# Kernel optimization log

Measured on AMD Instinct MI355X. Metric: run time of the kernel, lower is better.

The kernel has to match this reference:

```python
import jax, jax.numpy as jnp
import numpy as np

N = 200000   # 10000 graphs x 20 nodes, stacked
E = 3200000  # avg degree 16
F_IN = 4
H = 32
BN_EPS = 1e-5


def setup_inputs() -> dict:
    key = jax.random.key(0)
    ks = jax.random.split(key, 16)
    s = 0.1
    return {
        "x": jax.random.normal(ks[0], (N, F_IN), jnp.float32),
        "edge_index": jax.random.randint(ks[1], (2, E), 0, N, jnp.int64),
        "edge_weight": jax.random.uniform(ks[2], (E,), jnp.float32),
        "gcn1_w": jax.random.normal(ks[3], (F_IN, H), jnp.float32) * s,
        "gcn1_b": jnp.zeros((H,), jnp.float32),
        "gcn2_w": jax.random.normal(ks[4], (H, H), jnp.float32) * s,
        "gcn2_b": jnp.zeros((H,), jnp.float32),
        "bn1_gamma": jnp.ones((H,), jnp.float32),
        "bn1_beta": jnp.zeros((H,), jnp.float32),
        "bn1_mean": jnp.zeros((H,), jnp.float32),
        "bn1_var": jnp.ones((H,), jnp.float32),
        "bn2_gamma": jnp.ones((H,), jnp.float32),
        "bn2_beta": jnp.zeros((H,), jnp.float32),
        "bn2_mean": jnp.zeros((H,), jnp.float32),
        "bn2_var": jnp.ones((H,), jnp.float32),
        "lstm1_wih": jax.random.normal(ks[5], (4 * H, 2 * H), jnp.float32) * s,
        "lstm1_whh": jax.random.normal(ks[6], (4 * H, H), jnp.float32) * s,
        "lstm1_bih": jax.random.normal(ks[7], (4 * H,), jnp.float32) * s,
        "lstm1_bhh": jax.random.normal(ks[8], (4 * H,), jnp.float32) * s,
        "lstm2_wih": jax.random.normal(ks[9], (4 * H, H), jnp.float32) * s,
        "lstm2_whh": jax.random.normal(ks[10], (4 * H, H), jnp.float32) * s,
        "lstm2_bih": jax.random.normal(ks[11], (4 * H,), jnp.float32) * s,
        "lstm2_bhh": jax.random.normal(ks[12], (4 * H,), jnp.float32) * s,
        "lin_w": jax.random.normal(ks[13], (1, 2 * H + F_IN), jnp.float32) * s,
        "lin_b": jnp.zeros((1,), jnp.float32),
    }


def _gcn_conv(x, src, dst, ew, W, b, n):
    # GCNConv: x @ W, add self-loops (weight 1), symmetric normalization, scatter-add at dst.
    xw = x @ W
    loop = jnp.arange(n)
    s = jnp.concatenate([src, loop])
    d = jnp.concatenate([dst, loop])
    w = jnp.concatenate([ew, jnp.ones((n,), ew.dtype)])
    deg = jax.ops.segment_sum(w, d, num_segments=n)
    dinv = jnp.where(deg > 0, jax.lax.rsqrt(deg), 0.0)
    norm = dinv[s] * w * dinv[d]  # [E+N]
    out = jax.ops.segment_sum(norm[:, None] * xw[s], d, num_segments=n)
    return out + b


def _bn_eval(x, gamma, beta, mean, var):
    return (x - mean) * jax.lax.rsqrt(var + BN_EPS) * gamma + beta


def _lstm_step(x, wih, bih, bhh):
    # single timestep, zero initial (h, c): recurrent W_hh term vanishes.
    gates = x @ wih.T + bih + bhh
    i, f, g, o = jnp.split(gates, 4, axis=1)  # torch gate order i,f,g,o
    c = jax.nn.sigmoid(i) * jnp.tanh(g)
    return jax.nn.sigmoid(o) * jnp.tanh(c)


def reference(x, edge_index, edge_weight, gcn1_w, gcn1_b, gcn2_w, gcn2_b,
              bn1_gamma, bn1_beta, bn1_mean, bn1_var,
              bn2_gamma, bn2_beta, bn2_mean, bn2_var,
              lstm1_wih, lstm1_whh, lstm1_bih, lstm1_bhh,
              lstm2_wih, lstm2_whh, lstm2_bih, lstm2_bhh,
              lin_w, lin_b):
    n = x.shape[0]
    src, dst = edge_index[0], edge_index[1]
    # MPNNLSTM (window=1, eval mode: dropout=identity, BN uses running stats)
    h1 = _bn_eval(jax.nn.relu(_gcn_conv(x, src, dst, edge_weight, gcn1_w, gcn1_b, n)),
                  bn1_gamma, bn1_beta, bn1_mean, bn1_var)
    h2 = _bn_eval(jax.nn.relu(_gcn_conv(h1, src, dst, edge_weight, gcn2_w, gcn2_b, n)),
                  bn2_gamma, bn2_beta, bn2_mean, bn2_var)
    skip = jnp.concatenate([h1, h2], axis=1)  # [N, 2H]
    H1 = _lstm_step(skip, lstm1_wih, lstm1_bih, lstm1_bhh)  # [N, H]
    H2 = _lstm_step(H1, lstm2_wih, lstm2_bih, lstm2_bhh)    # [N, H]
    h = jnp.concatenate([H1, H2, x], axis=1)  # [N, 2H + F_IN]
    # RecurrentGCN head: relu + linear -> [N, 1]
    return jax.nn.relu(h) @ lin_w.T + lin_b
```

## Files before the change

kernel.cpp:

```cpp
#include <hip/hip_runtime.h>
#include <hip/hip_fp16.h>
#include <math.h>

#define BN_EPS 1e-5f
#define HF 32
#define BS 256
#define KEDGE 4096
#define MAXNB 800
#define WQ14 16383.0f
#define WQ22 4194303.0f

typedef _Float16 half8 __attribute__((ext_vector_type(8)));
typedef float f32x4 __attribute__((ext_vector_type(4)));
typedef float f32x2 __attribute__((ext_vector_type(2)));

__device__ __forceinline__ float fsig(float x) {
    return __builtin_amdgcn_rcpf(1.0f + __expf(-x));
}
__device__ __forceinline__ float ftanh(float x) {
    return 1.0f - 2.0f * __builtin_amdgcn_rcpf(1.0f + __expf(2.0f * x));
}


__device__ __forceinline__ float e4m3_to_f32_sw(unsigned v) {
    unsigned s = v & 0x80u, E = (v >> 3) & 0xFu, m = v & 7u;
    float r = E ? ldexpf((float)(8 + m), (int)E - 10) : ldexpf((float)m, -9);
    return s ? -r : r;
}

__device__ __forceinline__ unsigned f32_to_e4m3_sw(float x) {
    float ax = fabsf(x);
    unsigned s = x < 0.0f ? 0x80u : 0u;
    if (!(ax > 0.0f)) return s;
    if (ax >= 448.0f) return s | 0x7Eu;
    int e;
    float m = frexpf(ax, &e);
    int E = e - 1 + 7;
    if (E >= 1) {
        int q = (int)(m * 16.0f + 0.5f);
        if (q == 16) { q = 8; E += 1; if (E > 15) return s | 0x7Eu; }
        return s | (unsigned)(E << 3) | (unsigned)(q - 8);
    }
    int q = (int)(ax * 512.0f + 0.5f);
    if (q > 7) return s | 0x08u;
    return s | (unsigned)q;
}

__device__ __forceinline__ void dec8(uint2 r, float* f) {
#if __has_builtin(__builtin_amdgcn_cvt_pk_f32_fp8)
    f32x2 p0 = __builtin_amdgcn_cvt_pk_f32_fp8((int)r.x, false);
    f32x2 p1 = __builtin_amdgcn_cvt_pk_f32_fp8((int)r.x, true);
    f32x2 p2 = __builtin_amdgcn_cvt_pk_f32_fp8((int)r.y, false);
    f32x2 p3 = __builtin_amdgcn_cvt_pk_f32_fp8((int)r.y, true);
    f[0] = p0[0]; f[1] = p0[1]; f[2] = p1[0]; f[3] = p1[1];
    f[4] = p2[0]; f[5] = p2[1]; f[6] = p3[0]; f[7] = p3[1];
#else
#pragma unroll
    for (int k = 0; k < 4; ++k) f[k] = e4m3_to_f32_sw((r.x >> (8 * k)) & 0xFFu);
#pragma unroll
    for (int k = 0; k < 4; ++k) f[4 + k] = e4m3_to_f32_sw((r.y >> (8 * k)) & 0xFFu);
#endif
}

__device__ __forceinline__ uint2 enc8(const float* o) {
#if __has_builtin(__builtin_amdgcn_cvt_pk_fp8_f32)
    int w0 = 0, w1 = 0;
    w0 = __builtin_amdgcn_cvt_pk_fp8_f32(o[0], o[1], w0, false);
    w0 = __builtin_amdgcn_cvt_pk_fp8_f32(o[2], o[3], w0, true);
    w1 = __builtin_amdgcn_cvt_pk_fp8_f32(o[4], o[5], w1, false);
    w1 = __builtin_amdgcn_cvt_pk_fp8_f32(o[6], o[7], w1, true);
    return make_uint2((unsigned)w0, (unsigned)w1);
#else
    unsigned a = 0, b = 0;
#pragma unroll
    for (int k = 0; k < 4; ++k) a |= f32_to_e4m3_sw(o[k]) << (8 * k);
#pragma unroll
    for (int k = 0; k < 4; ++k) b |= f32_to_e4m3_sw(o[4 + k]) << (8 * k);
    return make_uint2(a, b);
#endif
}


__global__ __launch_bounds__(512) void k_binsort(
        const int* __restrict__ src, const int* __restrict__ dst,
        const float* __restrict__ ew, int E, int NB, int bcap,
        int* __restrict__ gcur, uint2* __restrict__ recs) {
    __shared__ uint2 srec[KEDGE];
    __shared__ int hist[MAXNB], excl[MAXNB], curs[MAXNB], sbase[MAXNB];

    int tid = threadIdx.x;
    int base = blockIdx.x * KEDGE;
    int cnt = min(KEDGE, E - base);

    for (int i = tid; i < NB; i += 512) hist[i] = 0;
    __syncthreads();

    for (int i = tid; i < cnt; i += 512)
        atomicAdd(&hist[dst[base + i] >> 8], 1);
    __syncthreads();

    if (tid < 64) {
        int run = 0;
        for (int c = 0; c < NB; c += 64) {
            int idx = c + tid;
            int v = (idx < NB) ? hist[idx] : 0;
            int incl = v;
#pragma unroll
            for (int o = 1; o < 64; o <<= 1) {
                int up = __shfl_up(incl, o, 64);
                if (tid >= o) incl += up;
            }
            if (idx < NB) { int e = run + incl - v; excl[idx] = e; curs[idx] = e; }
            run += __shfl(incl, 63, 64);
        }
    }
    __syncthreads();

    for (int i = tid; i < cnt; i += 512) {
        int s = src[base + i];
        int d = dst[base + i];
        float w = ew[base + i];
        unsigned q = (unsigned)(w * WQ22 + 0.5f);
        if (q > 4194303u) q = 4194303u;
        int b = d >> 8;
        int pos = atomicAdd(&curs[b], 1);
        srec[pos] = make_uint2(((unsigned)s << 8) | (unsigned)(d & 255),
                               ((unsigned)b << 22) | q);
    }
    __syncthreads();

    for (int b = tid; b < NB; b += 512) {
        int len = hist[b];
        sbase[b] = len ? atomicAdd(&gcur[b], len) : 0;
    }
    __syncthreads();

    for (int i = tid; i < cnt; i += 512) {
        uint2 u = srec[i];
        int b = u.y >> 22;
        int off = sbase[b] + (i - excl[b]);
        if (off < bcap) recs[(size_t)b * bcap + off] = u;
    }
}


__global__ __launch_bounds__(512) void k_sortb(
        const uint2* __restrict__ recs, const int* __restrict__ gcur, int bcap,
        unsigned* __restrict__ recs4, int* __restrict__ pstart,
        int* __restrict__ pcnt, float* __restrict__ dinv, int n) {
    __shared__ int hist[BS], excl[BS], curs[BS];
    __shared__ float wsum[BS];

    int b = blockIdx.x, tid = threadIdx.x;
    int cnt = min(gcur[b], bcap);
    const uint2* r = recs + (size_t)b * bcap;
    const float dq = 1.0f / WQ22;

    if (tid < BS) { hist[tid] = 0; wsum[tid] = 1.0f; }
    __syncthreads();

    for (int i = tid; i < cnt; i += 512) {
        uint2 u = r[i];
        int dl = u.x & 255;
        atomicAdd(&hist[dl], 1);
        atomicAdd(&wsum[dl], (float)(u.y & 4194303u) * dq);
    }
    __syncthreads();

    if (tid < BS) wsum[tid] = rsqrtf(wsum[tid]);
    if (tid < 64) {
        int run = 0;
        for (int c = 0; c < BS; c += 64) {
            int idx = c + tid;
            int v = hist[idx];
            int incl = v;
#pragma unroll
            for (int o = 1; o < 64; o <<= 1) {
                int up = __shfl_up(incl, o, 64);
                if (tid >= o) incl += up;
            }
            int e = run + incl - v;
            excl[idx] = e; curs[idx] = e;
            run += __shfl(incl, 63, 64);
        }
    }
    __syncthreads();

    unsigned* out4 = recs4 + (size_t)b * bcap;
    for (int i = tid; i < cnt; i += 512) {
        uint2 u = r[i];
        int dl = u.x & 255;
        int pos = atomicAdd(&curs[dl], 1);
        float qn = (float)(u.y & 4194303u) * dq * wsum[dl];
        unsigned q = (unsigned)(qn * WQ14 + 0.5f);
        if (q > 16383u) q = 16383u;
        out4[pos] = ((u.x >> 8) << 14) | q;
    }

    if (tid < BS) {
        int g = b * BS + tid;
        if (g < n) {
            pstart[g] = b * bcap + excl[tid];
            pcnt[g] = hist[tid];
            dinv[g] = wsum[tid];
        }
    }
}


__global__ __launch_bounds__(256) void k_prep(
        const float* __restrict__ wih1, const float* __restrict__ bih1,
        const float* __restrict__ bhh1, const float* __restrict__ wih2,
        const float* __restrict__ bih2, const float* __restrict__ bhh2,
        __half* __restrict__ wp1, __half* __restrict__ wp2,
        float* __restrict__ bsum1, float* __restrict__ bsum2,
        int* __restrict__ gcur, int NB,
        const float* __restrict__ x, const float* __restrict__ W1,
        unsigned char* __restrict__ y18, int n) {
    const int tg[6] = {0, 16, 64, 80, 96, 112};
    __shared__ float sW[128];
    int tid = threadIdx.x;
    if (tid < 128) sW[tid] = W1[tid];
    __syncthreads();

    int idx = blockIdx.x * 256 + tid;
    if (idx < 6144) {
        int t = idx >> 10, rem = idx & 1023;
        int kc = rem >> 9, rem2 = rem & 511;
        int lane = rem2 >> 3, j = rem2 & 7;
        int g = tg[t] + (lane & 15);
        int k = kc * 32 + (lane >> 4) * 8 + j;
        wp1[idx] = __float2half(wih1[g * 64 + k]);
    } else if (idx < 9216) {
        int i2 = idx - 6144;
        int t = i2 >> 9, rem2 = i2 & 511;
        int lane = rem2 >> 3, j = rem2 & 7;
        int g = tg[t] + (lane & 15);
        int k = (lane >> 4) * 8 + j;
        wp2[i2] = __float2half(wih2[g * 32 + k]);
    } else if (idx < 9344) {
        int i = idx - 9216;
        bsum1[i] = bih1[i] + bhh1[i];
    } else if (idx < 9472) {
        int i = idx - 9344;
        bsum2[i] = bih2[i] + bhh2[i];
    } else if (idx < 9472 + NB) {
        gcur[idx - 9472] = 0;
    } else if (idx >= 16384) {
        int j = idx - 16384;
        int node = j >> 2, lane = j & 3;
        if (node < n) {
            float4 xv = *(const float4*)(x + (size_t)node * 4);
            int fq = lane * 8;
            float o[8];
#pragma unroll
            for (int k = 0; k < 8; ++k)
                o[k] = xv.x * sW[fq + k] + xv.y * sW[32 + fq + k] +
                       xv.z * sW[64 + fq + k] + xv.w * sW[96 + fq + k];
            ((uint2*)(y18 + ((size_t)node << 5)))[lane] = enc8(o);
        }
    }
}


__global__ __launch_bounds__(256) void k_g1w2(
        const unsigned* __restrict__ recs4, const int* __restrict__ pstart,
        const int* __restrict__ pcnt, const float* __restrict__ dinv,
        const unsigned char* __restrict__ y18, const float* __restrict__ W2,
        const float* __restrict__ bias, const float* __restrict__ gamma,
        const float* __restrict__ beta, const float* __restrict__ mean,
        const float* __restrict__ var,
        __half* __restrict__ skiph, unsigned char* __restrict__ A8, int n) {
    __shared__ float sW2[1024];
    __shared__ float sh1[64][33];
    int tid = threadIdx.x;
    for (int i = tid; i < 1024; i += 256) sW2[i] = W2[i];
    __syncthreads();

    int nl = tid >> 2;
    int g = blockIdx.x * 64 + nl;
    int lane = tid & 3;
    int fq = lane * 8;
    bool act = g < n;

    float acc[8];
#pragma unroll
    for (int k = 0; k < 8; ++k) acc[k] = 0.0f;

    if (act) {
        float dig = dinv[g];
        float sl = dig * dig;
        {
            uint2 sr = ((const uint2*)(y18 + ((size_t)g << 5)))[lane];
            float f[8];
            dec8(sr, f);
#pragma unroll
            for (int k = 0; k < 8; ++k) acc[k] = sl * f[k];
        }

        const float qs = 1.0f / WQ14;
        int cn = pcnt[g];
        const unsigned* r = recs4 + pstart[g];
        int e = 0;
        for (; e + 8 <= cn; e += 8) {
            unsigned u[8];
            uint2 rw[8];
            float nm[8];
#pragma unroll
            for (int q = 0; q < 8; ++q) u[q] = r[e + q];
#pragma unroll
            for (int q = 0; q < 8; ++q)
                rw[q] = ((const uint2*)(y18 + ((size_t)(u[q] >> 14) << 5)))[lane];
#pragma unroll
            for (int q = 0; q < 8; ++q)
                nm[q] = (float)(u[q] & 16383u) * qs * dinv[u[q] >> 14];
#pragma unroll
            for (int q = 0; q < 8; ++q) {
                float f[8];
                dec8(rw[q], f);
#pragma unroll
                for (int k = 0; k < 8; ++k) acc[k] += nm[q] * f[k];
            }
        }
        for (; e < cn; ++e) {
            unsigned u0 = r[e];
            uint2 r0 = ((const uint2*)(y18 + ((size_t)(u0 >> 14) << 5)))[lane];
            float n0 = (float)(u0 & 16383u) * qs * dinv[u0 >> 14];
            float f[8];
            dec8(r0, f);
#pragma unroll
            for (int k = 0; k < 8; ++k) acc[k] += n0 * f[k];
        }
    }

    float o[8];
#pragma unroll
    for (int k = 0; k < 8; ++k) {
        float v = fmaxf(acc[k] + bias[fq + k], 0.0f);
        o[k] = (v - mean[fq + k]) * gamma[fq + k] * rsqrtf(var[fq + k] + BN_EPS) + beta[fq + k];
        sh1[nl][fq + k] = o[k];
    }
    if (act) {
        union { __half h[8]; uint4 q; } hv;
#pragma unroll
        for (int k = 0; k < 8; ++k) hv.h[k] = __float2half(o[k]);
        *(uint4*)(skiph + (size_t)g * 64 + fq) = hv.q;
    }
    __syncthreads();

    if (act) {
        float a2[8];
#pragma unroll
        for (int j = 0; j < 8; ++j) a2[j] = 0.0f;
#pragma unroll 4
        for (int k = 0; k < 32; ++k) {
            float h = sh1[nl][k];
            const float* wr = sW2 + k * 32 + fq;
#pragma unroll
            for (int j = 0; j < 8; ++j) a2[j] += h * wr[j];
        }
        ((uint2*)(A8 + ((size_t)g << 5)))[lane] = enc8(a2);
    }
}


__global__ __launch_bounds__(256) void k_gather8(
        const unsigned* __restrict__ recs4, const int* __restrict__ pstart,
        const int* __restrict__ pcnt, const float* __restrict__ dinv,
        const unsigned char* __restrict__ A8,
        const float* __restrict__ bias, const float* __restrict__ gamma,
        const float* __restrict__ beta, const float* __restrict__ mean,
        const float* __restrict__ var,
        __half* __restrict__ skiph, int uoff, int n) {
    int g = blockIdx.x * 64 + (threadIdx.x >> 2);
    int lane = threadIdx.x & 3;
    if (g >= n) return;

    float dig = dinv[g];
    float sl = dig * dig;
    float acc[8];
    {
        uint2 sr = ((const uint2*)(A8 + ((size_t)g << 5)))[lane];
        float f[8];
        dec8(sr, f);
#pragma unroll
        for (int k = 0; k < 8; ++k) acc[k] = sl * f[k];
    }

    const float qs = 1.0f / WQ14;
    int cn = pcnt[g];
    const unsigned* r = recs4 + pstart[g];
    int e = 0;
    for (; e + 8 <= cn; e += 8) {
        unsigned u[8];
        uint2 rw[8];
        float nm[8];
#pragma unroll
        for (int q = 0; q < 8; ++q) u[q] = r[e + q];
#pragma unroll
        for (int q = 0; q < 8; ++q)
            rw[q] = ((const uint2*)(A8 + ((size_t)(u[q] >> 14) << 5)))[lane];
#pragma unroll
        for (int q = 0; q < 8; ++q)
            nm[q] = (float)(u[q] & 16383u) * qs * dinv[u[q] >> 14];
#pragma unroll
        for (int q = 0; q < 8; ++q) {
            float f[8];
            dec8(rw[q], f);
#pragma unroll
            for (int k = 0; k < 8; ++k) acc[k] += nm[q] * f[k];
        }
    }
    for (; e < cn; ++e) {
        unsigned u0 = r[e];
        uint2 r0 = ((const uint2*)(A8 + ((size_t)(u0 >> 14) << 5)))[lane];
        float n0 = (float)(u0 & 16383u) * qs * dinv[u0 >> 14];
        float f0[8];
        dec8(r0, f0);
#pragma unroll
        for (int k = 0; k < 8; ++k) acc[k] += n0 * f0[k];
    }

    int fq = lane * 8;
    union { __half h[8]; uint4 q; } hv;
#pragma unroll
    for (int k = 0; k < 8; ++k) {
        float v = fmaxf(acc[k] + bias[fq + k], 0.0f);
        hv.h[k] = __float2half((v - mean[fq + k]) * gamma[fq + k] * rsqrtf(var[fq + k] + BN_EPS) + beta[fq + k]);
    }
    *(uint4*)(skiph + (size_t)g * 64 + uoff + fq) = hv.q;
}


__global__ __launch_bounds__(256) void k_headm(
        const __half* __restrict__ skiph, const float* __restrict__ x,
        const __half* __restrict__ wp1, const __half* __restrict__ wp2,
        const float* __restrict__ bsum1, const float* __restrict__ bsum2,
        const float* __restrict__ lw, const float* __restrict__ lb,
        float* __restrict__ out, int n) {
    __shared__ __align__(16) __half H1lds[4 * 16 * 40];
    int tid = threadIdx.x;
    int w = tid >> 6, l = tid & 63;
    int quad = l >> 4, c = l & 15;
    int node_base = blockIdx.x * 64 + w * 16;

    int arow = node_base + c; if (arow > n - 1) arow = n - 1;
    const half8* ap = (const half8*)(skiph + (size_t)arow * 64);
    half8 a0 = ap[quad];
    half8 a1 = ap[4 + quad];

    const half8* b1 = (const half8*)wp1;
    f32x4 d[6];
#pragma unroll
    for (int t = 0; t < 6; ++t) {
        f32x4 acc = {0.0f, 0.0f, 0.0f, 0.0f};
        acc = __builtin_amdgcn_mfma_f32_16x16x32_f16(a0, b1[(t * 2 + 0) * 64 + l], acc, 0, 0, 0);
        acc = __builtin_amdgcn_mfma_f32_16x16x32_f16(a1, b1[(t * 2 + 1) * 64 + l], acc, 0, 0, 0);
        d[t] = acc;
    }

    float bi0 = bsum1[c],      bi1 = bsum1[16 + c];
    float bg0 = bsum1[64 + c], bg1 = bsum1[80 + c];
    float bo0 = bsum1[96 + c], bo1 = bsum1[112 + c];
    float lwc0 = lw[c], lwc1 = lw[c + 16];

    float pa[4];
#pragma unroll
    for (int r = 0; r < 4; ++r) {
        float cc0 = fsig(d[0][r] + bi0) * ftanh(d[2][r] + bg0);
        float h0 = fsig(d[4][r] + bo0) * ftanh(cc0);
        float cc1 = fsig(d[1][r] + bi1) * ftanh(d[3][r] + bg1);
        float h1 = fsig(d[5][r] + bo1) * ftanh(cc1);
        pa[r] = fmaxf(h0, 0.0f) * lwc0 + fmaxf(h1, 0.0f) * lwc1;
        __half* hp = H1lds + (w * 16 + quad * 4 + r) * 40;
        hp[c] = __float2half(h0);
        hp[c + 16] = __float2half(h1);
    }
    __syncthreads();

    half8 a2 = *(const half8*)(H1lds + (w * 16 + c) * 40 + quad * 8);

    const half8* b2 = (const half8*)wp2;
    f32x4 e[6];
#pragma unroll
    for (int t = 0; t < 6; ++t) {
        f32x4 acc = {0.0f, 0.0f, 0.0f, 0.0f};
        e[t] = __builtin_amdgcn_mfma_f32_16x16x32_f16(a2, b2[t * 64 + l], acc, 0, 0, 0);
    }

    float ci0 = bsum2[c],      ci1 = bsum2[16 + c];
    float cg0 = bsum2[64 + c], cg1 = bsum2[80 + c];
    float co0 = bsum2[96 + c], co1 = bsum2[112 + c];
    float lw2c0 = lw[32 + c], lw2c1 = lw[48 + c];
#pragma unroll
    for (int r = 0; r < 4; ++r) {
        float cc0 = fsig(e[0][r] + ci0) * ftanh(e[2][r] + cg0);
        float h0 = fsig(e[4][r] + co0) * ftanh(cc0);
        float cc1 = fsig(e[1][r] + ci1) * ftanh(e[3][r] + cg1);
        float h1 = fsig(e[5][r] + co1) * ftanh(cc1);
        pa[r] += fmaxf(h0, 0.0f) * lw2c0 + fmaxf(h1, 0.0f) * lw2c1;
    }

#pragma unroll
    for (int m = 1; m < 16; m <<= 1) {
#pragma unroll
        for (int r = 0; r < 4; ++r) pa[r] += __shfl_xor(pa[r], m, 64);
    }

    if (c < 4) {
        int node = node_base + quad * 4 + c;
        if (node < n) {
            const float4 xv = *(const float4*)(x + (size_t)node * 4);
            out[node] = pa[c] + lb[0]
                + fmaxf(xv.x, 0.0f) * lw[64] + fmaxf(xv.y, 0.0f) * lw[65]
                + fmaxf(xv.z, 0.0f) * lw[66] + fmaxf(xv.w, 0.0f) * lw[67];
        }
    }
}


__global__ void k_initdeg(float* __restrict__ deg, int n) {
    int i = blockIdx.x * blockDim.x + threadIdx.x;
    if (i < n) deg[i] = 1.0f;
}

__global__ void k_deg_only(const int* __restrict__ dst, const float* __restrict__ ew,
                           float* __restrict__ deg, int E) {
    int e = blockIdx.x * blockDim.x + threadIdx.x;
    if (e < E) atomicAdd(&deg[dst[e]], ew[e]);
}

__global__ void k_dinv_f(float* __restrict__ deg, int n) {
    int i = blockIdx.x * blockDim.x + threadIdx.x;
    if (i < n) {
        float d = deg[i];
        deg[i] = d > 0.0f ? rsqrtf(d) : 0.0f;
    }
}

__global__ void k_xw1_f(const float* __restrict__ x, const float* __restrict__ W,
                        float* __restrict__ out, int n) {
    int idx = blockIdx.x * blockDim.x + threadIdx.x;
    if (idx >= n * HF) return;
    int nn = idx >> 5, f = idx & 31;
    const float4 xr = *(const float4*)(x + (size_t)nn * 4);
    out[idx] = xr.x * W[f] + xr.y * W[32 + f] + xr.z * W[64 + f] + xr.w * W[96 + f];
}

__global__ void k_xw2_f(const float* __restrict__ Hin, const float* __restrict__ W,
                        float* __restrict__ out, int n) {
    __shared__ float sW[32 * 32];
    __shared__ float sH[8][32];
    int tid = threadIdx.x;
    for (int i = tid; i < 1024; i += 256) sW[i] = W[i];
    int r = tid >> 5, f = tid & 31;
    int nn = blockIdx.x * 8 + r;
    if (nn < n) sH[r][f] = Hin[(size_t)nn * HF + f];
    __syncthreads();
    if (nn >= n) return;
    float acc = 0.0f;
#pragma unroll
    for (int k = 0; k < 32; ++k) acc += sH[r][k] * sW[k * 32 + f];
    out[(size_t)nn * HF + f] = acc;
}

__global__ void k_selfloop(const float* __restrict__ A, const float* __restrict__ dinv,
                           float* __restrict__ B, int n) {
    int idx = blockIdx.x * blockDim.x + threadIdx.x;
    if (idx >= n * HF) return;
    int nn = idx >> 5;
    float di = dinv[nn];
    B[idx] = di * di * A[idx];
}

__global__ void k_scatter(const int* __restrict__ src, const int* __restrict__ dst,
                          const float* __restrict__ ew, const float* __restrict__ dinv,
                          const float* __restrict__ A, float* __restrict__ B, int total) {
    int idx = blockIdx.x * blockDim.x + threadIdx.x;
    if (idx >= total) return;
    int e = idx >> 5, f = idx & 31;
    int s = src[e], d = dst[e];
    float norm = dinv[s] * ew[e] * dinv[d];
    atomicAdd(&B[d * HF + f], norm * A[s * HF + f]);
}

__global__ void k_post(const float* __restrict__ B, const float* __restrict__ bias,
                       const float* __restrict__ gamma, const float* __restrict__ beta,
                       const float* __restrict__ mean, const float* __restrict__ var,
                       float* __restrict__ Hout, int n) {
    int idx = blockIdx.x * blockDim.x + threadIdx.x;
    if (idx >= n * HF) return;
    int f = idx & 31;
    float v = fmaxf(B[idx] + bias[f], 0.0f);
    float sc = gamma[f] * rsqrtf(var[f] + BN_EPS);
    Hout[idx] = (v - mean[f]) * sc + beta[f];
}

__global__ __launch_bounds__(256) void k_head(
        const float* __restrict__ h1, const float* __restrict__ h2,
        const float* __restrict__ x,
        const float* __restrict__ wih1, const float* __restrict__ bih1, const float* __restrict__ bhh1,
        const float* __restrict__ wih2, const float* __restrict__ bih2, const float* __restrict__ bhh2,
        const float* __restrict__ lw, const float* __restrict__ lb,
        float* __restrict__ out, int n) {
    __shared__ float sH1[32 * 256];
    int tid = threadIdx.x;
    int nn = blockIdx.x * 256 + tid;
    if (nn >= n) return;

    const float4* a = (const float4*)(h1 + (size_t)nn * HF);
    const float4* b = (const float4*)(h2 + (size_t)nn * HF);
    float skip[64];
#pragma unroll
    for (int q = 0; q < 8; ++q) {
        float4 v = a[q];
        skip[4 * q] = v.x; skip[4 * q + 1] = v.y; skip[4 * q + 2] = v.z; skip[4 * q + 3] = v.w;
        float4 u = b[q];
        skip[32 + 4 * q] = u.x; skip[33 + 4 * q] = u.y; skip[34 + 4 * q] = u.z; skip[35 + 4 * q] = u.w;
    }

    float oa = lb[0];
#pragma unroll 1
    for (int j = 0; j < 32; ++j) {
        const float4* wi = (const float4*)(wih1 + (size_t)j * 64);
        const float4* wg = (const float4*)(wih1 + (size_t)(64 + j) * 64);
        const float4* wo = (const float4*)(wih1 + (size_t)(96 + j) * 64);
        float gi = bih1[j] + bhh1[j];
        float gg = bih1[64 + j] + bhh1[64 + j];
        float go = bih1[96 + j] + bhh1[96 + j];
#pragma unroll
        for (int q = 0; q < 16; ++q) {
            float4 aa = wi[q], bb = wg[q], cc4 = wo[q];
            float s0 = skip[4 * q], s1 = skip[4 * q + 1], s2 = skip[4 * q + 2], s3 = skip[4 * q + 3];
            gi += aa.x * s0 + aa.y * s1 + aa.z * s2 + aa.w * s3;
            gg += bb.x * s0 + bb.y * s1 + bb.z * s2 + bb.w * s3;
            go += cc4.x * s0 + cc4.y * s1 + cc4.z * s2 + cc4.w * s3;
        }
        float cc = fsig(gi) * ftanh(gg);
        float hh = fsig(go) * ftanh(cc);
        sH1[j * 256 + tid] = hh;
        oa += fmaxf(hh, 0.0f) * lw[j];
    }

#pragma unroll 1
    for (int j = 0; j < 32; ++j) {
        const float4* wi = (const float4*)(wih2 + (size_t)j * 32);
        const float4* wg = (const float4*)(wih2 + (size_t)(64 + j) * 32);
        const float4* wo = (const float4*)(wih2 + (size_t)(96 + j) * 32);
        float gi = bih2[j] + bhh2[j];
        float gg = bih2[64 + j] + bhh2[64 + j];
        float go = bih2[96 + j] + bhh2[96 + j];
#pragma unroll
        for (int q = 0; q < 8; ++q) {
            float4 aa = wi[q], bb = wg[q], cc4 = wo[q];
            float s0 = sH1[(4 * q) * 256 + tid], s1 = sH1[(4 * q + 1) * 256 + tid];
            float s2 = sH1[(4 * q + 2) * 256 + tid], s3 = sH1[(4 * q + 3) * 256 + tid];
            gi += aa.x * s0 + aa.y * s1 + aa.z * s2 + aa.w * s3;
            gg += bb.x * s0 + bb.y * s1 + bb.z * s2 + bb.w * s3;
            go += cc4.x * s0 + cc4.y * s1 + cc4.z * s2 + cc4.w * s3;
        }
        float cc = fsig(gi) * ftanh(gg);
        float hh = fsig(go) * ftanh(cc);
        oa += fmaxf(hh, 0.0f) * lw[32 + j];
    }

    const float4 xv = *(const float4*)(x + (size_t)nn * 4);
    oa += fmaxf(xv.x, 0.0f) * lw[64] + fmaxf(xv.y, 0.0f) * lw[65] +
          fmaxf(xv.z, 0.0f) * lw[66] + fmaxf(xv.w, 0.0f) * lw[67];
    out[nn] = oa;
}


extern "C" void kernel_launch(void* const* d_in, const int* in_sizes, int n_in,
                              void* d_out, int out_size, void* d_ws, size_t ws_size,
                              hipStream_t stream) {
    const float* x   = (const float*)d_in[0];
    const int*   ei  = (const int*)d_in[1];
    const float* ew  = (const float*)d_in[2];
    const float* g1w = (const float*)d_in[3];
    const float* g1b = (const float*)d_in[4];
    const float* g2w = (const float*)d_in[5];
    const float* g2b = (const float*)d_in[6];
    const float* bn1g = (const float*)d_in[7];
    const float* bn1b = (const float*)d_in[8];
    const float* bn1m = (const float*)d_in[9];
    const float* bn1v = (const float*)d_in[10];
    const float* bn2g = (const float*)d_in[11];
    const float* bn2b = (const float*)d_in[12];
    const float* bn2m = (const float*)d_in[13];
    const float* bn2v = (const float*)d_in[14];
    const float* w1ih = (const float*)d_in[15];
    const float* b1ih = (const float*)d_in[17];
    const float* b1hh = (const float*)d_in[18];
    const float* w2ih = (const float*)d_in[19];
    const float* b2ih = (const float*)d_in[21];
    const float* b2hh = (const float*)d_in[22];
    const float* lw   = (const float*)d_in[23];
    const float* lb   = (const float*)d_in[24];
    float* out = (float*)d_out;

    const int N = in_sizes[0] / 4;
    const int E = in_sizes[2];
    const int* src = ei;
    const int* dst = ei + E;

    const int T = 256;
    const int NB = (N + BS - 1) / BS;
    long long meanb = ((long long)BS * E) / (N > 0 ? N : 1);
    int bcap = (int)(meanb + meanb / 4 + 128);

    char* p = (char*)d_ws;
    auto alloc = [&](size_t bytes) { char* q = p; p += (bytes + 255) & ~(size_t)255; return q; };
    int*      gcur   = (int*)alloc(sizeof(int) * NB);
    uint2*    recs   = (uint2*)alloc(sizeof(uint2) * (size_t)NB * bcap);
    unsigned* recs4  = (unsigned*)alloc(sizeof(unsigned) * (size_t)NB * bcap);
    float*    dinv   = (float*)alloc(sizeof(float) * N);
    int*      pstart = (int*)alloc(sizeof(int) * N);
    int*      pcnt   = (int*)alloc(sizeof(int) * N);
    unsigned char* y18 = (unsigned char*)alloc((size_t)N * HF);
    unsigned char* A8  = (unsigned char*)alloc((size_t)N * HF);
    __half*   skiph  = (__half*)alloc(sizeof(__half) * (size_t)N * 64);
    __half*   wp1    = (__half*)alloc(sizeof(__half) * 6144);
    __half*   wp2    = (__half*)alloc(sizeof(__half) * 3072);
    float*    bsum1  = (float*)alloc(sizeof(float) * 128);
    float*    bsum2  = (float*)alloc(sizeof(float) * 128);
    size_t need = (size_t)(p - (char*)d_ws);

    int bN  = (N + T - 1) / T;
    int bE  = (E + T - 1) / T;
    int bNF = (N * HF + T - 1) / T;
    int bN8 = (N + 7) / 8;
    int bG  = (N + 63) / 64;
    int bBin = (E + KEDGE - 1) / KEDGE;
    int bPrep = (16384 + 4 * N + 255) / 256;

    if (ws_size >= need && NB <= MAXNB && N <= (1 << 18)) {
        k_prep<<<bPrep, 256, 0, stream>>>(w1ih, b1ih, b1hh, w2ih, b2ih, b2hh,
                                          wp1, wp2, bsum1, bsum2, gcur, NB,
                                          x, g1w, y18, N);
        k_binsort<<<bBin, 512, 0, stream>>>(src, dst, ew, E, NB, bcap, gcur, recs);
        k_sortb<<<NB, 512, 0, stream>>>(recs, gcur, bcap, recs4, pstart, pcnt, dinv, N);

        k_g1w2<<<bG, T, 0, stream>>>(recs4, pstart, pcnt, dinv, y18, g2w,
                                     g1b, bn1g, bn1b, bn1m, bn1v, skiph, A8, N);
        k_gather8<<<bG, T, 0, stream>>>(recs4, pstart, pcnt, dinv, A8,
                                        g2b, bn2g, bn2b, bn2m, bn2v, skiph, 32, N);
        k_headm<<<bG, T, 0, stream>>>(skiph, x, wp1, wp2, bsum1, bsum2,
                                      lw, lb, out, N);
    } else {
        size_t Npad = ((size_t)N + 255) & ~(size_t)255;
        float* fdinv = (float*)d_ws;
        float* fA = fdinv + Npad;
        float* fB = fA + (size_t)N * HF;
        float* fC = fB + (size_t)N * HF;
        int bEF = (int)(((long long)E * HF + T - 1) / T);
        int bH = (N + 255) / 256;

        k_initdeg<<<bN, T, 0, stream>>>(fdinv, N);
        k_deg_only<<<bE, T, 0, stream>>>(dst, ew, fdinv, E);
        k_dinv_f<<<bN, T, 0, stream>>>(fdinv, N);

        k_xw1_f<<<bNF, T, 0, stream>>>(x, g1w, fA, N);
        k_selfloop<<<bNF, T, 0, stream>>>(fA, fdinv, fB, N);
        k_scatter<<<bEF, T, 0, stream>>>(src, dst, ew, fdinv, fA, fB, E * HF);
        k_post<<<bNF, T, 0, stream>>>(fB, g1b, bn1g, bn1b, bn1m, bn1v, fC, N);

        k_xw2_f<<<bN8, T, 0, stream>>>(fC, g2w, fA, N);
        k_selfloop<<<bNF, T, 0, stream>>>(fA, fdinv, fB, N);
        k_scatter<<<bEF, T, 0, stream>>>(src, dst, ew, fdinv, fA, fB, E * HF);
        k_post<<<bNF, T, 0, stream>>>(fB, g2b, bn2g, bn2b, bn2m, bn2v, fB, N);

        k_head<<<bH, T, 0, stream>>>(fC, fB, x, w1ih, b1ih, b1hh, w2ih, b2ih, b2hh,
                                     lw, lb, out, N);
    }
}
```

Before: 332.0 us.

## Degree-sort nodes within buckets, pad CSR rows for vector loads, global weight sums

Builds a per-bucket permutation that groups nodes by in-degree, so the gather kernels process nodes of similar degree together and wavefronts diverge less. Pads each node's CSR segment to a multiple of four so edge records can be read with uint4 loads. The weighted-degree sum now comes from integer global atomics in the binning kernel instead of a second pass in k_sortb. In exchange it adds a global atomic per edge, a perm indirection, extra workspace and a serial prefix sum in each sort block.

```diff
diff --git a/kernel.cpp b/kernel.cpp
--- a/kernel.cpp
+++ b/kernel.cpp
@@ -84,7 +84,8 @@
 __global__ __launch_bounds__(512) void k_binsort(
         const int* __restrict__ src, const int* __restrict__ dst,
         const float* __restrict__ ew, int E, int NB, int bcap,
-        int* __restrict__ gcur, uint2* __restrict__ recs) {
+        int* __restrict__ gcur, uint2* __restrict__ recs,
+        int* __restrict__ wsumi) {
     __shared__ uint2 srec[KEDGE];
     __shared__ int hist[MAXNB], excl[MAXNB], curs[MAXNB], sbase[MAXNB];
 
@@ -122,6 +123,7 @@
         float w = ew[base + i];
         unsigned q = (unsigned)(w * WQ22 + 0.5f);
         if (q > 4194303u) q = 4194303u;
+        atomicAdd(&wsumi[d], (int)q);
         int b = d >> 8;
         int pos = atomicAdd(&curs[b], 1);
         srec[pos] = make_uint2(((unsigned)s << 8) | (unsigned)(d & 255),
@@ -145,34 +147,37 @@
 
 
 __global__ __launch_bounds__(512) void k_sortb(
-        const uint2* __restrict__ recs, const int* __restrict__ gcur, int bcap,
+        const uint2* __restrict__ recs, const int* __restrict__ gcur,
+        int bcap, int bcap4, const int* __restrict__ wsumi,
         unsigned* __restrict__ recs4, int* __restrict__ pstart,
-        int* __restrict__ pcnt, float* __restrict__ dinv, int n) {
-    __shared__ int hist[BS], excl[BS], curs[BS];
-    __shared__ float wsum[BS];
+        int* __restrict__ pcnt, float* __restrict__ dinv,
+        int* __restrict__ perm, int n) {
+    __shared__ int hist[BS], excl4[BS], curs[BS];
+    __shared__ float sdv[BS];
+    __shared__ int dh[66];
 
     int b = blockIdx.x, tid = threadIdx.x;
     int cnt = min(gcur[b], bcap);
     const uint2* r = recs + (size_t)b * bcap;
     const float dq = 1.0f / WQ22;
 
-    if (tid < BS) { hist[tid] = 0; wsum[tid] = 1.0f; }
-    __syncthreads();
-
-    for (int i = tid; i < cnt; i += 512) {
-        uint2 u = r[i];
-        int dl = u.x & 255;
-        atomicAdd(&hist[dl], 1);
-        atomicAdd(&wsum[dl], (float)(u.y & 4194303u) * dq);
-    }
-    __syncthreads();
-
-    if (tid < BS) wsum[tid] = rsqrtf(wsum[tid]);
+    if (tid < BS) hist[tid] = 0;
+    if (tid < 66) dh[tid] = 0;
+    __syncthreads();
+
+    for (int i = tid; i < cnt; i += 512)
+        atomicAdd(&hist[r[i].x & 255], 1);
+    __syncthreads();
+
+    if (tid < BS) {
+        int g = b * BS + tid;
+        sdv[tid] = (g < n) ? rsqrtf(1.0f + (float)wsumi[g] * dq) : 0.0f;
+    }
     if (tid < 64) {
         int run = 0;
         for (int c = 0; c < BS; c += 64) {
             int idx = c + tid;
-            int v = hist[idx];
+            int v = (hist[idx] + 3) & ~3;
             int incl = v;
 #pragma unroll
             for (int o = 1; o < 64; o <<= 1) {
@@ -180,18 +185,18 @@
                 if (tid >= o) incl += up;
             }
             int e = run + incl - v;
-            excl[idx] = e; curs[idx] = e;
+            excl4[idx] = e; curs[idx] = e;
             run += __shfl(incl, 63, 64);
         }
     }
     __syncthreads();
 
-    unsigned* out4 = recs4 + (size_t)b * bcap;
+    unsigned* out4 = recs4 + (size_t)b * bcap4;
     for (int i = tid; i < cnt; i += 512) {
         uint2 u = r[i];
         int dl = u.x & 255;
         int pos = atomicAdd(&curs[dl], 1);
-        float qn = (float)(u.y & 4194303u) * dq * wsum[dl];
+        float qn = (float)(u.y & 4194303u) * dq * sdv[dl];
         unsigned q = (unsigned)(qn * WQ14 + 0.5f);
         if (q > 16383u) q = 16383u;
         out4[pos] = ((u.x >> 8) << 14) | q;
@@ -199,10 +204,24 @@
 
     if (tid < BS) {
         int g = b * BS + tid;
+        int key = (g < n) ? min(hist[tid], 63) : 64;
+        atomicAdd(&dh[key + 1], 1);
+    }
+    __syncthreads();
+    if (tid == 0) {
+#pragma unroll 1
+        for (int k = 1; k < 66; ++k) dh[k] += dh[k - 1];
+    }
+    __syncthreads();
+    if (tid < BS) {
+        int g = b * BS + tid;
+        int key = (g < n) ? min(hist[tid], 63) : 64;
+        int pos = atomicAdd(&dh[key], 1);
+        perm[b * BS + pos] = g;
         if (g < n) {
-            pstart[g] = b * bcap + excl[tid];
+            pstart[g] = b * bcap4 + excl4[tid];
             pcnt[g] = hist[tid];
-            dinv[g] = wsum[tid];
+            dinv[g] = sdv[tid];
         }
     }
 }
@@ -216,7 +235,7 @@
         float* __restrict__ bsum1, float* __restrict__ bsum2,
         int* __restrict__ gcur, int NB,
         const float* __restrict__ x, const float* __restrict__ W1,
-        unsigned char* __restrict__ y18, int n) {
+        unsigned char* __restrict__ y18, int* __restrict__ wsumi, int n) {
     const int tg[6] = {0, 16, 64, 80, 96, 112};
     __shared__ float sW[128];
     int tid = threadIdx.x;
@@ -248,8 +267,8 @@
         gcur[idx - 9472] = 0;
     } else if (idx >= 16384) {
         int j = idx - 16384;
-        int node = j >> 2, lane = j & 3;
-        if (node < n) {
+        if (j < 4 * n) {
+            int node = j >> 2, lane = j & 3;
             float4 xv = *(const float4*)(x + (size_t)node * 4);
             int fq = lane * 8;
             float o[8];
@@ -258,6 +277,8 @@
                 o[k] = xv.x * sW[fq + k] + xv.y * sW[32 + fq + k] +
                        xv.z * sW[64 + fq + k] + xv.w * sW[96 + fq + k];
             ((uint2*)(y18 + ((size_t)node << 5)))[lane] = enc8(o);
+        } else if (j < 5 * n) {
+            wsumi[j - 4 * n] = 0;
         }
     }
 }
@@ -266,6 +287,7 @@
 __global__ __launch_bounds__(256) void k_g1w2(
         const unsigned* __restrict__ recs4, const int* __restrict__ pstart,
         const int* __restrict__ pcnt, const float* __restrict__ dinv,
+        const int* __restrict__ perm,
         const unsigned char* __restrict__ y18, const float* __restrict__ W2,
         const float* __restrict__ bias, const float* __restrict__ gamma,
         const float* __restrict__ beta, const float* __restrict__ mean,
@@ -278,7 +300,7 @@
     __syncthreads();
 
     int nl = tid >> 2;
-    int g = blockIdx.x * 64 + nl;
+    int g = perm[blockIdx.x * 64 + nl];
     int lane = tid & 3;
     int fq = lane * 8;
     bool act = g < n;
@@ -303,11 +325,11 @@
         const unsigned* r = recs4 + pstart[g];
         int e = 0;
         for (; e + 8 <= cn; e += 8) {
-            unsigned u[8];
+            uint4 ua = *(const uint4*)(r + e);
+            uint4 ub = *(const uint4*)(r + e + 4);
+            unsigned u[8] = {ua.x, ua.y, ua.z, ua.w, ub.x, ub.y, ub.z, ub.w};
             uint2 rw[8];
             float nm[8];
-#pragma unroll
-            for (int q = 0; q < 8; ++q) u[q] = r[e + q];
 #pragma unroll
             for (int q = 0; q < 8; ++q)
                 rw[q] = ((const uint2*)(y18 + ((size_t)(u[q] >> 14) << 5)))[lane];
@@ -367,12 +389,13 @@
 __global__ __launch_bounds__(256) void k_gather8(
         const unsigned* __restrict__ recs4, const int* __restrict__ pstart,
         const int* __restrict__ pcnt, const float* __restrict__ dinv,
+        const int* __restrict__ perm,
         const unsigned char* __restrict__ A8,
         const float* __restrict__ bias, const float* __restrict__ gamma,
         const float* __restrict__ beta, const float* __restrict__ mean,
         const float* __restrict__ var,
         __half* __restrict__ skiph, int uoff, int n) {
-    int g = blockIdx.x * 64 + (threadIdx.x >> 2);
+    int g = perm[blockIdx.x * 64 + (threadIdx.x >> 2)];
     int lane = threadIdx.x & 3;
     if (g >= n) return;
 
@@ -392,11 +415,11 @@
     const unsigned* r = recs4 + pstart[g];
     int e = 0;
     for (; e + 8 <= cn; e += 8) {
-        unsigned u[8];
+        uint4 ua = *(const uint4*)(r + e);
+        uint4 ub = *(const uint4*)(r + e + 4);
+        unsigned u[8] = {ua.x, ua.y, ua.z, ua.w, ub.x, ub.y, ub.z, ub.w};
         uint2 rw[8];
         float nm[8];
-#pragma unroll
-        for (int q = 0; q < 8; ++q) u[q] = r[e + q];
 #pragma unroll
         for (int q = 0; q < 8; ++q)
             rw[q] = ((const uint2*)(A8 + ((size_t)(u[q] >> 14) << 5)))[lane];
@@ -708,15 +731,19 @@
     const int NB = (N + BS - 1) / BS;
     long long meanb = ((long long)BS * E) / (N > 0 ? N : 1);
     int bcap = (int)(meanb + meanb / 4 + 128);
+    bcap = (bcap + 3) & ~3;
+    int bcap4 = bcap + 3 * BS;
 
     char* p = (char*)d_ws;
     auto alloc = [&](size_t bytes) { char* q = p; p += (bytes + 255) & ~(size_t)255; return q; };
     int*      gcur   = (int*)alloc(sizeof(int) * NB);
     uint2*    recs   = (uint2*)alloc(sizeof(uint2) * (size_t)NB * bcap);
-    unsigned* recs4  = (unsigned*)alloc(sizeof(unsigned) * (size_t)NB * bcap);
+    unsigned* recs4  = (unsigned*)alloc(sizeof(unsigned) * (size_t)NB * bcap4);
+    int*      wsumi  = (int*)alloc(sizeof(int) * N);
     float*    dinv   = (float*)alloc(sizeof(float) * N);
     int*      pstart = (int*)alloc(sizeof(int) * N);
     int*      pcnt   = (int*)alloc(sizeof(int) * N);
+    int*      perm   = (int*)alloc(sizeof(int) * (size_t)NB * BS);
     unsigned char* y18 = (unsigned char*)alloc((size_t)N * HF);
     unsigned char* A8  = (unsigned char*)alloc((size_t)N * HF);
     __half*   skiph  = (__half*)alloc(sizeof(__half) * (size_t)N * 64);
@@ -731,20 +758,22 @@
     int bNF = (N * HF + T - 1) / T;
     int bN8 = (N + 7) / 8;
     int bG  = (N + 63) / 64;
+    int bG4 = NB * 4;
     int bBin = (E + KEDGE - 1) / KEDGE;
-    int bPrep = (16384 + 4 * N + 255) / 256;
+    int bPrep = (16384 + 5 * N + 255) / 256;
 
     if (ws_size >= need && NB <= MAXNB && N <= (1 << 18)) {
         k_prep<<<bPrep, 256, 0, stream>>>(w1ih, b1ih, b1hh, w2ih, b2ih, b2hh,
                                           wp1, wp2, bsum1, bsum2, gcur, NB,
-                                          x, g1w, y18, N);
-        k_binsort<<<bBin, 512, 0, stream>>>(src, dst, ew, E, NB, bcap, gcur, recs);
-        k_sortb<<<NB, 512, 0, stream>>>(recs, gcur, bcap, recs4, pstart, pcnt, dinv, N);
-
-        k_g1w2<<<bG, T, 0, stream>>>(recs4, pstart, pcnt, dinv, y18, g2w,
-                                     g1b, bn1g, bn1b, bn1m, bn1v, skiph, A8, N);
-        k_gather8<<<bG, T, 0, stream>>>(recs4, pstart, pcnt, dinv, A8,
-                                        g2b, bn2g, bn2b, bn2m, bn2v, skiph, 32, N);
+                                          x, g1w, y18, wsumi, N);
+        k_binsort<<<bBin, 512, 0, stream>>>(src, dst, ew, E, NB, bcap, gcur, recs, wsumi);
+        k_sortb<<<NB, 512, 0, stream>>>(recs, gcur, bcap, bcap4, wsumi,
+                                        recs4, pstart, pcnt, dinv, perm, N);
+
+        k_g1w2<<<bG4, T, 0, stream>>>(recs4, pstart, pcnt, dinv, perm, y18, g2w,
+                                      g1b, bn1g, bn1b, bn1m, bn1v, skiph, A8, N);
+        k_gather8<<<bG4, T, 0, stream>>>(recs4, pstart, pcnt, dinv, perm, A8,
+                                         g2b, bn2g, bn2b, bn2m, bn2v, skiph, 32, N);
         k_headm<<<bG, T, 0, stream>>>(skiph, x, wp1, wp2, bsum1, bsum2,
                                       lw, lb, out, N);
     } else {
```

Result: slower. 457.3 us (+37.8%).

## Fold source dinv into stored features and vectorize edge record loads

Applied to the files above, without the earlier changes.

Source-side normalization dinv[src] is now folded into the gathered feature tables: the layer-1 projection x@W1 is computed in the sort kernel and pre-scaled by dinv, and the layer-2 A8 features are pre-scaled by dinv before encoding. This removes one random dinv gather per edge in both aggregation passes. Per-node edge lists are padded to multiples of four so records can be read as aligned uint4 loads. Weight sums are accumulated as integers, which changes rounding slightly, and quantizing pre-scaled features may affect precision.

```diff
diff --git a/kernel.cpp b/kernel.cpp
--- a/kernel.cpp
+++ b/kernel.cpp
@@ -145,34 +145,42 @@
 
 
 __global__ __launch_bounds__(512) void k_sortb(
-        const uint2* __restrict__ recs, const int* __restrict__ gcur, int bcap,
+        const uint2* __restrict__ recs, const int* __restrict__ gcur,
+        int bcap, int bcap4,
+        const float* __restrict__ x, const float* __restrict__ W1,
         unsigned* __restrict__ recs4, int* __restrict__ pstart,
-        int* __restrict__ pcnt, float* __restrict__ dinv, int n) {
-    __shared__ int hist[BS], excl[BS], curs[BS];
-    __shared__ float wsum[BS];
+        int* __restrict__ pcnt, float* __restrict__ dinv,
+        unsigned char* __restrict__ y18, int n) {
+    __shared__ int hist[BS], excl4[BS], curs[BS], wsm[BS];
+    __shared__ float sdv[BS];
+    __shared__ float sW1[128];
 
     int b = blockIdx.x, tid = threadIdx.x;
     int cnt = min(gcur[b], bcap);
     const uint2* r = recs + (size_t)b * bcap;
     const float dq = 1.0f / WQ22;
 
-    if (tid < BS) { hist[tid] = 0; wsum[tid] = 1.0f; }
+    if (tid < BS) { hist[tid] = 0; wsm[tid] = 0; }
+    if (tid >= 256 && tid < 384) sW1[tid - 256] = W1[tid - 256];
     __syncthreads();
 
     for (int i = tid; i < cnt; i += 512) {
         uint2 u = r[i];
         int dl = u.x & 255;
         atomicAdd(&hist[dl], 1);
-        atomicAdd(&wsum[dl], (float)(u.y & 4194303u) * dq);
-    }
-    __syncthreads();
-
-    if (tid < BS) wsum[tid] = rsqrtf(wsum[tid]);
+        atomicAdd(&wsm[dl], (int)(u.y & 4194303u));
+    }
+    __syncthreads();
+
+    if (tid < BS) {
+        int g = b * BS + tid;
+        sdv[tid] = (g < n) ? rsqrtf(1.0f + (float)wsm[tid] * dq) : 0.0f;
+    }
     if (tid < 64) {
         int run = 0;
         for (int c = 0; c < BS; c += 64) {
             int idx = c + tid;
-            int v = hist[idx];
+            int v = (hist[idx] + 3) & ~3;
             int incl = v;
 #pragma unroll
             for (int o = 1; o < 64; o <<= 1) {
@@ -180,29 +188,46 @@
                 if (tid >= o) incl += up;
             }
             int e = run + incl - v;
-            excl[idx] = e; curs[idx] = e;
+            excl4[idx] = e; curs[idx] = e;
             run += __shfl(incl, 63, 64);
         }
     }
     __syncthreads();
 
-    unsigned* out4 = recs4 + (size_t)b * bcap;
+    unsigned* out4 = recs4 + (size_t)b * bcap4;
     for (int i = tid; i < cnt; i += 512) {
         uint2 u = r[i];
         int dl = u.x & 255;
         int pos = atomicAdd(&curs[dl], 1);
-        float qn = (float)(u.y & 4194303u) * dq * wsum[dl];
+        float qn = (float)(u.y & 4194303u) * dq * sdv[dl];
         unsigned q = (unsigned)(qn * WQ14 + 0.5f);
         if (q > 16383u) q = 16383u;
         out4[pos] = ((u.x >> 8) << 14) | q;
     }
 
+    {
+        int node = tid >> 1, half = tid & 1;
+        int g = b * BS + node;
+        if (g < n) {
+            float4 xv = *(const float4*)(x + (size_t)g * 4);
+            float sc = sdv[node];
+            int f0 = half * 16;
+            float o[16];
+#pragma unroll
+            for (int k = 0; k < 16; ++k)
+                o[k] = sc * (xv.x * sW1[f0 + k] + xv.y * sW1[32 + f0 + k] +
+                             xv.z * sW1[64 + f0 + k] + xv.w * sW1[96 + f0 + k]);
+            uint2 lo = enc8(o), hi = enc8(o + 8);
+            *(uint4*)(y18 + ((size_t)g << 5) + half * 16) = make_uint4(lo.x, lo.y, hi.x, hi.y);
+        }
+    }
+
     if (tid < BS) {
         int g = b * BS + tid;
         if (g < n) {
-            pstart[g] = b * bcap + excl[tid];
+            pstart[g] = b * bcap4 + excl4[tid];
             pcnt[g] = hist[tid];
-            dinv[g] = wsum[tid];
+            dinv[g] = sdv[tid];
         }
     }
 }
@@ -214,16 +239,9 @@
         const float* __restrict__ bih2, const float* __restrict__ bhh2,
         __half* __restrict__ wp1, __half* __restrict__ wp2,
         float* __restrict__ bsum1, float* __restrict__ bsum2,
-        int* __restrict__ gcur, int NB,
-        const float* __restrict__ x, const float* __restrict__ W1,
-        unsigned char* __restrict__ y18, int n) {
+        int* __restrict__ gcur, int NB) {
     const int tg[6] = {0, 16, 64, 80, 96, 112};
-    __shared__ float sW[128];
-    int tid = threadIdx.x;
-    if (tid < 128) sW[tid] = W1[tid];
-    __syncthreads();
-
-    int idx = blockIdx.x * 256 + tid;
+    int idx = blockIdx.x * 256 + threadIdx.x;
     if (idx < 6144) {
         int t = idx >> 10, rem = idx & 1023;
         int kc = rem >> 9, rem2 = rem & 511;
@@ -246,19 +264,6 @@
         bsum2[i] = bih2[i] + bhh2[i];
     } else if (idx < 9472 + NB) {
         gcur[idx - 9472] = 0;
-    } else if (idx >= 16384) {
-        int j = idx - 16384;
-        int node = j >> 2, lane = j & 3;
-        if (node < n) {
-            float4 xv = *(const float4*)(x + (size_t)node * 4);
-            int fq = lane * 8;
-            float o[8];
-#pragma unroll
-            for (int k = 0; k < 8; ++k)
-                o[k] = xv.x * sW[fq + k] + xv.y * sW[32 + fq + k] +
-                       xv.z * sW[64 + fq + k] + xv.w * sW[96 + fq + k];
-            ((uint2*)(y18 + ((size_t)node << 5)))[lane] = enc8(o);
-        }
     }
 }
 
@@ -287,15 +292,15 @@
 #pragma unroll
     for (int k = 0; k < 8; ++k) acc[k] = 0.0f;
 
+    float dig = 0.0f;
     if (act) {
-        float dig = dinv[g];
-        float sl = dig * dig;
+        dig = dinv[g];
         {
             uint2 sr = ((const uint2*)(y18 + ((size_t)g << 5)))[lane];
             float f[8];
             dec8(sr, f);
 #pragma unroll
-            for (int k = 0; k < 8; ++k) acc[k] = sl * f[k];
+            for (int k = 0; k < 8; ++k) acc[k] = dig * f[k];
         }
 
         const float qs = 1.0f / WQ14;
@@ -303,17 +308,17 @@
         const unsigned* r = recs4 + pstart[g];
         int e = 0;
         for (; e + 8 <= cn; e += 8) {
-            unsigned u[8];
+            uint4 ua = *(const uint4*)(r + e);
+            uint4 ub = *(const uint4*)(r + e + 4);
+            unsigned u[8] = {ua.x, ua.y, ua.z, ua.w, ub.x, ub.y, ub.z, ub.w};
             uint2 rw[8];
-            float nm[8];
-#pragma unroll
-            for (int q = 0; q < 8; ++q) u[q] = r[e + q];
 #pragma unroll
             for (int q = 0; q < 8; ++q)
                 rw[q] = ((const uint2*)(y18 + ((size_t)(u[q] >> 14) << 5)))[lane];
+            float nm[8];
 #pragma unroll
             for (int q = 0; q < 8; ++q)
-                nm[q] = (float)(u[q] & 16383u) * qs * dinv[u[q] >> 14];
+                nm[q] = (float)(u[q] & 16383u) * qs;
 #pragma unroll
             for (int q = 0; q < 8; ++q) {
                 float f[8];
@@ -325,7 +330,7 @@
         for (; e < cn; ++e) {
             unsigned u0 = r[e];
             uint2 r0 = ((const uint2*)(y18 + ((size_t)(u0 >> 14) << 5)))[lane];
-            float n0 = (float)(u0 & 16383u) * qs * dinv[u0 >> 14];
+            float n0 = (float)(u0 & 16383u) * qs;
             float f[8];
             dec8(r0, f);
 #pragma unroll
@@ -359,6 +364,8 @@
 #pragma unroll
             for (int j = 0; j < 8; ++j) a2[j] += h * wr[j];
         }
+#pragma unroll
+        for (int j = 0; j < 8; ++j) a2[j] *= dig;
         ((uint2*)(A8 + ((size_t)g << 5)))[lane] = enc8(a2);
     }
 }
@@ -377,14 +384,13 @@
     if (g >= n) return;
 
     float dig = dinv[g];
-    float sl = dig * dig;
     float acc[8];
     {
         uint2 sr = ((const uint2*)(A8 + ((size_t)g << 5)))[lane];
         float f[8];
         dec8(sr, f);
 #pragma unroll
-        for (int k = 0; k < 8; ++k) acc[k] = sl * f[k];
+        for (int k = 0; k < 8; ++k) acc[k] = dig * f[k];
     }
 
     const float qs = 1.0f / WQ14;
@@ -392,17 +398,17 @@
     const unsigned* r = recs4 + pstart[g];
     int e = 0;
     for (; e + 8 <= cn; e += 8) {
-        unsigned u[8];
+        uint4 ua = *(const uint4*)(r + e);
+        uint4 ub = *(const uint4*)(r + e + 4);
+        unsigned u[8] = {ua.x, ua.y, ua.z, ua.w, ub.x, ub.y, ub.z, ub.w};
         uint2 rw[8];
-        float nm[8];
-#pragma unroll
-        for (int q = 0; q < 8; ++q) u[q] = r[e + q];
 #pragma unroll
         for (int q = 0; q < 8; ++q)
             rw[q] = ((const uint2*)(A8 + ((size_t)(u[q] >> 14) << 5)))[lane];
+        float nm[8];
 #pragma unroll
         for (int q = 0; q < 8; ++q)
-            nm[q] = (float)(u[q] & 16383u) * qs * dinv[u[q] >> 14];
+            nm[q] = (float)(u[q] & 16383u) * qs;
 #pragma unroll
         for (int q = 0; q < 8; ++q) {
             float f[8];
@@ -414,7 +420,7 @@
     for (; e < cn; ++e) {
         unsigned u0 = r[e];
         uint2 r0 = ((const uint2*)(A8 + ((size_t)(u0 >> 14) << 5)))[lane];
-        float n0 = (float)(u0 & 16383u) * qs * dinv[u0 >> 14];
+        float n0 = (float)(u0 & 16383u) * qs;
         float f0[8];
         dec8(r0, f0);
 #pragma unroll
@@ -708,12 +714,14 @@
     const int NB = (N + BS - 1) / BS;
     long long meanb = ((long long)BS * E) / (N > 0 ? N : 1);
     int bcap = (int)(meanb + meanb / 4 + 128);
+    bcap = (bcap + 3) & ~3;
+    int bcap4 = bcap + 3 * BS;
 
     char* p = (char*)d_ws;
     auto alloc = [&](size_t bytes) { char* q = p; p += (bytes + 255) & ~(size_t)255; return q; };
     int*      gcur   = (int*)alloc(sizeof(int) * NB);
     uint2*    recs   = (uint2*)alloc(sizeof(uint2) * (size_t)NB * bcap);
-    unsigned* recs4  = (unsigned*)alloc(sizeof(unsigned) * (size_t)NB * bcap);
+    unsigned* recs4  = (unsigned*)alloc(sizeof(unsigned) * (size_t)NB * bcap4);
     float*    dinv   = (float*)alloc(sizeof(float) * N);
     int*      pstart = (int*)alloc(sizeof(int) * N);
     int*      pcnt   = (int*)alloc(sizeof(int) * N);
@@ -732,14 +740,14 @@
     int bN8 = (N + 7) / 8;
     int bG  = (N + 63) / 64;
     int bBin = (E + KEDGE - 1) / KEDGE;
-    int bPrep = (16384 + 4 * N + 255) / 256;
+    int bPrep = (9472 + NB + 255) / 256;
 
     if (ws_size >= need && NB <= MAXNB && N <= (1 << 18)) {
         k_prep<<<bPrep, 256, 0, stream>>>(w1ih, b1ih, b1hh, w2ih, b2ih, b2hh,
-                                          wp1, wp2, bsum1, bsum2, gcur, NB,
-                                          x, g1w, y18, N);
+                                          wp1, wp2, bsum1, bsum2, gcur, NB);
         k_binsort<<<bBin, 512, 0, stream>>>(src, dst, ew, E, NB, bcap, gcur, recs);
-        k_sortb<<<NB, 512, 0, stream>>>(recs, gcur, bcap, recs4, pstart, pcnt, dinv, N);
+        k_sortb<<<NB, 512, 0, stream>>>(recs, gcur, bcap, bcap4, x, g1w,
+                                        recs4, pstart, pcnt, dinv, y18, N);
 
         k_g1w2<<<bG, T, 0, stream>>>(recs4, pstart, pcnt, dinv, y18, g2w,
                                      g1b, bn1g, bn1b, bn1m, bn1v, skiph, A8, N);
```

Result: faster. 299.1 us (-9.9%).
